# Optimization experiments

Measured on AMD Instinct MI355X. Metric: run time of the kernel, lower is better.

Reference implementation:

```python
import jax, jax.numpy as jnp
import numpy as np

D = 1024      # n_embd
NH = 16       # attention heads
E = 8         # n_experts
K = 2         # k_best
FF = 4 * D    # expert MLP hidden
EPS = 1e-6    # rms_norm_epsilon
TEMP = 1.0    # target_temperature


def setup_inputs() -> dict:
    key = jax.random.key(0)
    ks = jax.random.split(key, 12)
    B, S = 2, 1024
    s = 0.02
    return {
        "x": jax.random.normal(ks[0], (B, S, D), jnp.float32),
        "attn_norm_w": jnp.ones((D,), jnp.float32),
        "wq": jax.random.normal(ks[1], (D, D), jnp.float32) * s,
        "wk": jax.random.normal(ks[2], (D, D), jnp.float32) * s,
        "wv": jax.random.normal(ks[3], (D, D), jnp.float32) * s,
        "wo": jax.random.normal(ks[4], (D, D), jnp.float32) * s,
        "mlp_norm_w": jnp.ones((D,), jnp.float32),
        "router_w": jax.random.normal(ks[5], (D, E), jnp.float32) * s,
        "w1": jax.random.normal(ks[6], (E, D, FF), jnp.float32) * s,
        "b1": jnp.zeros((E, FF), jnp.float32),
        "w2": jax.random.normal(ks[7], (E, FF, D), jnp.float32) * s,
        "b2": jnp.zeros((E, D), jnp.float32),
    }


def _rmsnorm(x, w):
    var = jnp.mean(jnp.square(x), axis=-1, keepdims=True)
    return x * jax.lax.rsqrt(var + EPS) * w


def _attention(x, wq, wk, wv, wo):
    B, S, _ = x.shape
    dh = D // NH
    q = (x @ wq).reshape(B, S, NH, dh)
    k = (x @ wk).reshape(B, S, NH, dh)
    v = (x @ wv).reshape(B, S, NH, dh)
    scores = jnp.einsum("bqhd,bkhd->bhqk", q, k) / jnp.sqrt(jnp.float32(dh))
    causal = jnp.tril(jnp.ones((S, S), bool))  # [S,S]
    scores = jnp.where(causal[None, None], scores, jnp.finfo(scores.dtype).min)
    attn = jax.nn.softmax(scores, axis=-1)
    out = jnp.einsum("bhqk,bkhd->bqhd", attn, v).reshape(B, S, D)
    return out @ wo


def reference(x, attn_norm_w, wq, wk, wv, wo, mlp_norm_w, router_w, w1, b1, w2, b2):
    B, S, _ = x.shape
    # attention sub-block
    x = x + _attention(_rmsnorm(x, attn_norm_w), wq, wk, wv, wo)
    residual = x
    h = _rmsnorm(x, mlp_norm_w)  # [B,S,D]

    # router: temperature softmax + top-k
    logits = h @ router_w / TEMP                      # [B,S,E]
    probs = jax.nn.softmax(logits, axis=-1)
    top_k_scores, top_k_indices = jax.lax.top_k(probs, K)  # [B,S,K]
    onehot = jax.nn.one_hot(top_k_indices, E, dtype=h.dtype)  # [B,S,K,E]
    gates = jnp.einsum("bsk,bske->bse", top_k_scores, onehot)  # [B,S,E]

    # load-balancing loss (Switch-style) + expert counts
    counts = jnp.sum(onehot, axis=(0, 1, 2))          # [E]
    frac = counts / (B * S * K)
    mean_prob = jnp.mean(probs, axis=(0, 1))          # [E]
    balancing_loss = E * jnp.sum(frac * mean_prob)

    # experts: dense dispatch; tokens with zero gate contribute nothing,
    # so this matches the sort/gather/scatter top-k combine exactly.
    pre = jnp.einsum("bsd,edf->ebsf", h, w1) + b1[:, None, None]  # [E,B,S,FF]
    act = jax.nn.gelu(pre)
    y = jnp.einsum("ebsf,efd->ebsd", act, w2) + b2[:, None, None]  # [E,B,S,D]
    moe = jnp.einsum("ebsd,bse->bsd", y, gates)

    out = residual + moe
    return out, balancing_loss, counts
```

## Files before the change

kernel.cpp:

```cpp
#include <hip/hip_runtime.h>

typedef __bf16 bf16;
typedef __bf16 bf16x8 __attribute__((ext_vector_type(8)));
typedef float f32x4 __attribute__((ext_vector_type(4)));

#define D_   1024
#define S_   1024
#define B_   2
#define NTOK 2048
#define FF_  4096
#define NE   8
#define CAP  5120
#define OUTN 2097152

__device__ __forceinline__ float gelu_f(float x) {
    return 0.5f * x * (1.0f + tanhf(0.7978845608028654f * (x + 0.044715f * x * x * x)));
}

__global__ __launch_bounds__(256) void rmsnorm_k(const float* __restrict__ x,
                                                 const float* __restrict__ w,
                                                 float* __restrict__ yf,
                                                 bf16* __restrict__ yhi,
                                                 bf16* __restrict__ ylo) {
    int row = blockIdx.x;
    int t = threadIdx.x;
    const float* xr = x + (size_t)row * D_;
    float4 v = *(const float4*)(xr + t * 4);
    float ss = v.x * v.x + v.y * v.y + v.z * v.z + v.w * v.w;
    for (int off = 32; off; off >>= 1) ss += __shfl_down(ss, off);
    __shared__ float wsum[4];
    if ((t & 63) == 0) wsum[t >> 6] = ss;
    __syncthreads();
    float tot = wsum[0] + wsum[1] + wsum[2] + wsum[3];
    float rr = rsqrtf(tot * (1.0f / D_) + 1e-6f);
    float4 wv = *(const float4*)(w + t * 4);
    float y[4];
    y[0] = v.x * rr * wv.x; y[1] = v.y * rr * wv.y;
    y[2] = v.z * rr * wv.z; y[3] = v.w * rr * wv.w;
    if (yf) *(float4*)(yf + (size_t)row * D_ + t * 4) = *(float4*)y;
    if (yhi) {
#pragma unroll
        for (int i = 0; i < 4; i++) {
            bf16 hi = (bf16)y[i];
            yhi[(size_t)row * D_ + t * 4 + i] = hi;
            if (ylo) ylo[(size_t)row * D_ + t * 4 + i] = (bf16)(y[i] - (float)hi);
        }
    }
}

__global__ __launch_bounds__(256) void trans_split_k(
    const float* __restrict__ w0, const float* __restrict__ w1p,
    const float* __restrict__ w2p, const float* __restrict__ w3,
    bf16* o0h, bf16* o0l, bf16* o1h, bf16* o1l,
    bf16* o2h, bf16* o2l, bf16* o3h, bf16* o3l) {
    int z = blockIdx.z;
    const float* src = (z == 0) ? w0 : (z == 1) ? w1p : (z == 2) ? w2p : w3;
    bf16* dh = (z == 0) ? o0h : (z == 1) ? o1h : (z == 2) ? o2h : o3h;
    bf16* dl = (z == 0) ? o0l : (z == 1) ? o1l : (z == 2) ? o2l : o3l;
    __shared__ float tl[32][33];
    int c0 = blockIdx.x * 32, r0 = blockIdx.y * 32;
    int tx = threadIdx.x & 31, ty = threadIdx.x >> 5;
#pragma unroll
    for (int i = 0; i < 4; i++) {
        int r = ty + i * 8;
        tl[r][tx] = src[(size_t)(r0 + r) * 1024 + c0 + tx];
    }
    __syncthreads();
#pragma unroll
    for (int i = 0; i < 4; i++) {
        int c = ty + i * 8;
        float v = tl[tx][c];
        bf16 hi = (bf16)v;
        dh[(size_t)(c0 + c) * 1024 + r0 + tx] = hi;
        dl[(size_t)(c0 + c) * 1024 + r0 + tx] = (bf16)(v - (float)hi);
    }
}

__global__ __launch_bounds__(256) void transpose_cast_k(const float* __restrict__ in,
                                                        bf16* __restrict__ out,
                                                        int R, int C) {
    __shared__ float tl[32][33];
    size_t base = (size_t)blockIdx.z * R * C;
    const float* src = in + base;
    bf16* dst = out + base;
    int c0 = blockIdx.x * 32, r0 = blockIdx.y * 32;
    int tx = threadIdx.x & 31, tyy = threadIdx.x >> 5;
#pragma unroll
    for (int i = 0; i < 4; i++) {
        int r = tyy + i * 8;
        tl[r][tx] = src[(size_t)(r0 + r) * C + c0 + tx];
    }
    __syncthreads();
#pragma unroll
    for (int i = 0; i < 4; i++) {
        int c = tyy + i * 8;
        dst[(size_t)(c0 + c) * R + r0 + tx] = (bf16)tl[tx][c];
    }
}

#define GLD 40

#define GEMM64_SPLIT_BODY(N0EXPR, EPILOGUE)                                            \
    __shared__ bf16 Ash[64 * GLD], Asl[64 * GLD], Bsh[64 * GLD], Bsl[64 * GLD];        \
    int t = threadIdx.x;                                                               \
    int m0 = blockIdx.x * 64;                                                          \
    int n0 = (N0EXPR);                                                                 \
    int wv = t >> 6, ln = t & 63, l15 = ln & 15, qd = ln >> 4;                         \
    int srow = t >> 2, skc = (t & 3) * 8;                                              \
    f32x4 acc[4];                                                                      \
    _Pragma("unroll") for (int mt = 0; mt < 4; mt++) acc[mt] = (f32x4){0.f,0.f,0.f,0.f}; \
    for (int k0 = 0; k0 < 1024; k0 += 32) {                                            \
        __syncthreads();                                                               \
        *(bf16x8*)&Ash[srow * GLD + skc] = *(const bf16x8*)(Ah + (size_t)(m0 + srow) * 1024 + k0 + skc); \
        *(bf16x8*)&Asl[srow * GLD + skc] = *(const bf16x8*)(Al + (size_t)(m0 + srow) * 1024 + k0 + skc); \
        *(bf16x8*)&Bsh[srow * GLD + skc] = *(const bf16x8*)(Bh + (size_t)(n0 + srow) * 1024 + k0 + skc); \
        *(bf16x8*)&Bsl[srow * GLD + skc] = *(const bf16x8*)(Bl + (size_t)(n0 + srow) * 1024 + k0 + skc); \
        __syncthreads();                                                               \
        bf16x8 ah[4], al[4];                                                           \
        _Pragma("unroll") for (int mt = 0; mt < 4; mt++) {                             \
            ah[mt] = *(const bf16x8*)&Ash[(mt * 16 + l15) * GLD + qd * 8];             \
            al[mt] = *(const bf16x8*)&Asl[(mt * 16 + l15) * GLD + qd * 8];             \
        }                                                                              \
        bf16x8 bh = *(const bf16x8*)&Bsh[(wv * 16 + l15) * GLD + qd * 8];              \
        bf16x8 bl = *(const bf16x8*)&Bsl[(wv * 16 + l15) * GLD + qd * 8];              \
        _Pragma("unroll") for (int mt = 0; mt < 4; mt++) {                             \
            acc[mt] = __builtin_amdgcn_mfma_f32_16x16x32_bf16(ah[mt], bh, acc[mt], 0, 0, 0); \
            acc[mt] = __builtin_amdgcn_mfma_f32_16x16x32_bf16(ah[mt], bl, acc[mt], 0, 0, 0); \
            acc[mt] = __builtin_amdgcn_mfma_f32_16x16x32_bf16(al[mt], bh, acc[mt], 0, 0, 0); \
        }                                                                              \
    }                                                                                  \
    int gnl = wv * 16 + l15;                                                           \
    _Pragma("unroll") for (int mt = 0; mt < 4; mt++)                                   \
        _Pragma("unroll") for (int r = 0; r < 4; r++) {                                \
            int gm = m0 + mt * 16 + qd * 4 + r;                                        \
            float vv = acc[mt][r];                                                     \
            EPILOGUE                                                                   \
        }

__global__ __launch_bounds__(256) void gemm_qkv_k(
    const bf16* __restrict__ Ah, const bf16* __restrict__ Al,
    const bf16* __restrict__ Bqh, const bf16* __restrict__ Bql,
    const bf16* __restrict__ Bkh, const bf16* __restrict__ Bkl,
    const bf16* __restrict__ Bvh, const bf16* __restrict__ Bvl,
    bf16* Cqh, bf16* Cql, bf16* Ckh, bf16* Ckl, bf16* Cvh, bf16* Cvl) {
    int gy = blockIdx.y, zw = gy >> 4;
    const bf16* Bh = (zw == 0) ? Bqh : (zw == 1) ? Bkh : Bvh;
    const bf16* Bl = (zw == 0) ? Bql : (zw == 1) ? Bkl : Bvl;
    bf16* Ch = (zw == 0) ? Cqh : (zw == 1) ? Ckh : Cvh;
    bf16* Cl = (zw == 0) ? Cql : (zw == 1) ? Ckl : Cvl;
    GEMM64_SPLIT_BODY((gy & 15) * 64, {
        bf16 hi = (bf16)vv;
        Ch[(size_t)gm * D_ + n0 + gnl] = hi;
        Cl[(size_t)gm * D_ + n0 + gnl] = (bf16)(vv - (float)hi);
    })
}

__global__ __launch_bounds__(256) void gemm_wo_k(
    const bf16* __restrict__ Ah, const bf16* __restrict__ Al,
    const bf16* __restrict__ Bh, const bf16* __restrict__ Bl,
    float* __restrict__ C, const float* __restrict__ X) {
    GEMM64_SPLIT_BODY(blockIdx.y * 64, {
        C[(size_t)gm * D_ + n0 + gnl] = X[(size_t)gm * D_ + n0 + gnl] + vv;
    })
}

#define AP 72

__global__ __launch_bounds__(256) void attn_mfma_k(
    const bf16* __restrict__ qhp, const bf16* __restrict__ qlp,
    const bf16* __restrict__ khp, const bf16* __restrict__ klp,
    const bf16* __restrict__ vhp, const bf16* __restrict__ vlp,
    bf16* __restrict__ aoh, bf16* __restrict__ aol) {
    int qt = (int)gridDim.x - 1 - (int)blockIdx.x;
    int h = blockIdx.y, b = blockIdx.z;
    __shared__ bf16 Ksh[64 * AP], Ksl[64 * AP], VTh[64 * AP], VTl[64 * AP];
    __shared__ bf16 Ph[4][16 * AP], Pl[4][16 * AP];
    int t = threadIdx.x, wv = t >> 6, ln = t & 63, l15 = ln & 15, qd = ln >> 4;

    bf16x8 aqh[2], aql[2];
    {
        size_t qb = ((size_t)(b * S_ + qt * 64 + wv * 16 + l15)) * D_ + h * 64 + qd * 8;
        aqh[0] = *(const bf16x8*)(qhp + qb);
        aqh[1] = *(const bf16x8*)(qhp + qb + 32);
        aql[0] = *(const bf16x8*)(qlp + qb);
        aql[1] = *(const bf16x8*)(qlp + qb + 32);
    }
    f32x4 oacc[4];
    float mrow[4], lrow[4];
#pragma unroll
    for (int i = 0; i < 4; i++) {
        oacc[i] = (f32x4){0.f, 0.f, 0.f, 0.f};
        mrow[i] = -1e30f; lrow[i] = 0.0f;
    }

    for (int kt = 0; kt <= qt; kt++) {
        __syncthreads();
#pragma unroll
        for (int j = 0; j < 2; j++) {
            int idx = t + j * 256;
            int row = idx >> 3, ch = (idx & 7) * 8;
            size_t g = ((size_t)(b * S_ + kt * 64 + row)) * D_ + h * 64 + ch;
            *(bf16x8*)&Ksh[row * AP + ch] = *(const bf16x8*)(khp + g);
            *(bf16x8*)&Ksl[row * AP + ch] = *(const bf16x8*)(klp + g);
            bf16x8 vvh = *(const bf16x8*)(vhp + g);
            bf16x8 vvl = *(const bf16x8*)(vlp + g);
#pragma unroll
            for (int jj = 0; jj < 8; jj++) {
                VTh[(ch + jj) * AP + row] = vvh[jj];
                VTl[(ch + jj) * AP + row] = vvl[jj];
            }
        }
        __syncthreads();

        f32x4 sacc[4];
#pragma unroll
        for (int nt = 0; nt < 4; nt++) sacc[nt] = (f32x4){0.f, 0.f, 0.f, 0.f};
#pragma unroll
        for (int ks = 0; ks < 2; ks++) {
#pragma unroll
            for (int nt = 0; nt < 4; nt++) {
                bf16x8 bh = *(const bf16x8*)&Ksh[(nt * 16 + l15) * AP + ks * 32 + qd * 8];
                bf16x8 bl = *(const bf16x8*)&Ksl[(nt * 16 + l15) * AP + ks * 32 + qd * 8];
                sacc[nt] = __builtin_amdgcn_mfma_f32_16x16x32_bf16(aqh[ks], bh, sacc[nt], 0, 0, 0);
                sacc[nt] = __builtin_amdgcn_mfma_f32_16x16x32_bf16(aqh[ks], bl, sacc[nt], 0, 0, 0);
                sacc[nt] = __builtin_amdgcn_mfma_f32_16x16x32_bf16(aql[ks], bh, sacc[nt], 0, 0, 0);
            }
        }
        bool diag = (kt == qt);
#pragma unroll
        for (int r = 0; r < 4; r++) {
            float s0[4];
#pragma unroll
            for (int nt = 0; nt < 4; nt++) {
                s0[nt] = sacc[nt][r] * 0.125f;
                if (diag && (nt * 16 + l15) > (wv * 16 + qd * 4 + r)) s0[nt] = -1e30f;
            }
            float vmax = fmaxf(fmaxf(s0[0], s0[1]), fmaxf(s0[2], s0[3]));
            for (int off = 1; off < 16; off <<= 1) vmax = fmaxf(vmax, __shfl_xor(vmax, off));
            float mnew = fmaxf(mrow[r], vmax);
            float alpha = expf(mrow[r] - mnew);
            float p[4], rs = 0.0f;
#pragma unroll
            for (int nt = 0; nt < 4; nt++) { p[nt] = expf(s0[nt] - mnew); rs += p[nt]; }
            for (int off = 1; off < 16; off <<= 1) rs += __shfl_xor(rs, off);
            lrow[r] = lrow[r] * alpha + rs;
            mrow[r] = mnew;
#pragma unroll
            for (int nt = 0; nt < 4; nt++) oacc[nt][r] *= alpha;
            int prow = qd * 4 + r;
#pragma unroll
            for (int nt = 0; nt < 4; nt++) {
                bf16 hi = (bf16)p[nt];
                Ph[wv][prow * AP + nt * 16 + l15] = hi;
                Pl[wv][prow * AP + nt * 16 + l15] = (bf16)(p[nt] - (float)hi);
            }
        }
#pragma unroll
        for (int ks2 = 0; ks2 < 2; ks2++) {
            bf16x8 aph = *(const bf16x8*)&Ph[wv][l15 * AP + ks2 * 32 + qd * 8];
            bf16x8 apl = *(const bf16x8*)&Pl[wv][l15 * AP + ks2 * 32 + qd * 8];
#pragma unroll
            for (int nt = 0; nt < 4; nt++) {
                bf16x8 bvh = *(const bf16x8*)&VTh[(nt * 16 + l15) * AP + ks2 * 32 + qd * 8];
                bf16x8 bvl = *(const bf16x8*)&VTl[(nt * 16 + l15) * AP + ks2 * 32 + qd * 8];
                oacc[nt] = __builtin_amdgcn_mfma_f32_16x16x32_bf16(aph, bvh, oacc[nt], 0, 0, 0);
                oacc[nt] = __builtin_amdgcn_mfma_f32_16x16x32_bf16(aph, bvl, oacc[nt], 0, 0, 0);
                oacc[nt] = __builtin_amdgcn_mfma_f32_16x16x32_bf16(apl, bvh, oacc[nt], 0, 0, 0);
            }
        }
    }

#pragma unroll
    for (int r = 0; r < 4; r++) {
        float inv = 1.0f / lrow[r];
        size_t rowa = ((size_t)(b * S_ + qt * 64 + wv * 16 + qd * 4 + r)) * D_ + h * 64;
#pragma unroll
        for (int nt = 0; nt < 4; nt++) {
            float o = oacc[nt][r] * inv;
            bf16 hi = (bf16)o;
            aoh[rowa + nt * 16 + l15] = hi;
            aol[rowa + nt * 16 + l15] = (bf16)(o - (float)hi);
        }
    }
}

__global__ __launch_bounds__(256) void router_k(const float* __restrict__ h,
                                                const float* __restrict__ rw,
                                                int* __restrict__ tidx,
                                                float* __restrict__ tgate,
                                                int* __restrict__ ecnt,
                                                float* __restrict__ psum) {
    int wv = threadIdx.x >> 6, ln = threadIdx.x & 63;
    int tok = blockIdx.x * 4 + wv;
    const float* hr = h + (size_t)tok * D_;
    float acc[NE];
#pragma unroll
    for (int e = 0; e < NE; e++) acc[e] = 0.0f;
    int base = ln * 16;
#pragma unroll
    for (int c = 0; c < 4; c++) {
        float4 hv = *(const float4*)(hr + base + c * 4);
        const float* rp = rw + (size_t)(base + c * 4) * NE;
        float hx[4] = {hv.x, hv.y, hv.z, hv.w};
#pragma unroll
        for (int jj = 0; jj < 4; jj++)
#pragma unroll
            for (int e = 0; e < NE; e++)
                acc[e] = fmaf(hx[jj], rp[jj * NE + e], acc[e]);
    }
#pragma unroll
    for (int e = 0; e < NE; e++)
        for (int off = 32; off; off >>= 1) acc[e] += __shfl_down(acc[e], off);

    __shared__ float pb[4][NE];
    if (ln == 0) {
        float mx = acc[0];
#pragma unroll
        for (int e = 1; e < NE; e++) mx = fmaxf(mx, acc[e]);
        float p[NE], ssum = 0.0f;
#pragma unroll
        for (int e = 0; e < NE; e++) { p[e] = expf(acc[e] - mx); ssum += p[e]; }
        float inv = 1.0f / ssum;
#pragma unroll
        for (int e = 0; e < NE; e++) p[e] *= inv;
        int i0 = 0; float b0 = p[0];
#pragma unroll
        for (int e = 1; e < NE; e++) if (p[e] > b0) { b0 = p[e]; i0 = e; }
        int i1 = -1; float b1v = -1.0f;
#pragma unroll
        for (int e = 0; e < NE; e++) if (e != i0 && p[e] > b1v) { b1v = p[e]; i1 = e; }
        tidx[tok * 2] = i0; tidx[tok * 2 + 1] = i1;
        tgate[tok * 2] = b0; tgate[tok * 2 + 1] = b1v;
        atomicAdd(&ecnt[i0], 1);
        atomicAdd(&ecnt[i1], 1);
#pragma unroll
        for (int e = 0; e < NE; e++) pb[wv][e] = p[e];
    }
    __syncthreads();
    if (threadIdx.x < NE) {
        float s2 = pb[0][threadIdx.x] + pb[1][threadIdx.x] + pb[2][threadIdx.x] + pb[3][threadIdx.x];
        atomicAdd(&psum[threadIdx.x], s2);
    }
}

__global__ void passb_k(const int* __restrict__ ecnt, const float* __restrict__ psum,
                        int* __restrict__ eoffp, int* __restrict__ ecnt2,
                        float* __restrict__ out_tail) {
    if (threadIdx.x == 0) {
        int off = 0; float loss = 0.0f;
        for (int e = 0; e < NE; e++) {
            eoffp[e] = off;
            int c = ecnt[e];
            off += (c + 127) & ~127;
            loss += (c * (1.0f / 4096.0f)) * (psum[e] * (1.0f / 2048.0f));
            out_tail[1 + e] = (float)c;
            ecnt2[e] = 0;
        }
        eoffp[NE] = off;
        out_tail[0] = 8.0f * loss;
    }
}

__global__ __launch_bounds__(256) void scatter_k(const int* __restrict__ tidx,
                                                 const int* __restrict__ eoffp,
                                                 int* __restrict__ ecnt2,
                                                 int* __restrict__ stok,
                                                 int* __restrict__ sidx) {
    int tok = blockIdx.x * 256 + threadIdx.x;
    for (int k = 0; k < 2; k++) {
        int e = tidx[tok * 2 + k];
        int pos = eoffp[e] + atomicAdd(&ecnt2[e], 1);
        stok[pos] = tok;
        sidx[tok * 2 + k] = pos;
    }
}

#define MLD 40

__global__ __launch_bounds__(256) void moe_gemm1_k(const bf16* __restrict__ hB,
                                                   const bf16* __restrict__ w1t,
                                                   const float* __restrict__ b1,
                                                   const int* __restrict__ eoffp,
                                                   const int* __restrict__ stok,
                                                   bf16* __restrict__ act) {
    int m0 = blockIdx.x * 128, n0 = blockIdx.y * 128;
    if (m0 >= eoffp[NE]) return;
    int e = 0;
#pragma unroll
    for (int i = 1; i < NE; i++) if (m0 >= eoffp[i]) e = i;

    __shared__ bf16 As[128 * MLD];
    __shared__ bf16 Bs[128 * MLD];
    __shared__ int tok_l[128];
    int t = threadIdx.x;
    if (t < 128) tok_l[t] = stok[m0 + t];

    int wv = t >> 6, ln = t & 63;
    int wm = wv >> 1, wn = wv & 1;
    int lane15 = ln & 15, quad = ln >> 4;
    f32x4 acc[4][4];
#pragma unroll
    for (int mt = 0; mt < 4; mt++)
#pragma unroll
        for (int nt = 0; nt < 4; nt++) acc[mt][nt] = (f32x4){0.f, 0.f, 0.f, 0.f};

    const bf16* Bbase = w1t + ((size_t)e * FF_ + n0) * D_;

    for (int k0 = 0; k0 < D_; k0 += 32) {
        __syncthreads();
#pragma unroll
        for (int j = 0; j < 2; j++) {
            int idx = t + j * 256;
            int row = idx >> 2, kc = (idx & 3) * 8;
            uint4 av = *(const uint4*)(hB + (size_t)tok_l[row] * D_ + k0 + kc);
            *(uint4*)&As[row * MLD + kc] = av;
            uint4 bv = *(const uint4*)(Bbase + (size_t)row * D_ + k0 + kc);
            *(uint4*)&Bs[row * MLD + kc] = bv;
        }
        __syncthreads();
        bf16x8 af[4], bfr[4];
#pragma unroll
        for (int mt = 0; mt < 4; mt++)
            af[mt] = *(const bf16x8*)&As[(wm * 64 + mt * 16 + lane15) * MLD + quad * 8];
#pragma unroll
        for (int nt = 0; nt < 4; nt++)
            bfr[nt] = *(const bf16x8*)&Bs[(wn * 64 + nt * 16 + lane15) * MLD + quad * 8];
#pragma unroll
        for (int mt = 0; mt < 4; mt++)
#pragma unroll
            for (int nt = 0; nt < 4; nt++)
                acc[mt][nt] = __builtin_amdgcn_mfma_f32_16x16x32_bf16(af[mt], bfr[nt], acc[mt][nt], 0, 0, 0);
    }

    const float* b1e = b1 + (size_t)e * FF_;
#pragma unroll
    for (int mt = 0; mt < 4; mt++)
#pragma unroll
        for (int nt = 0; nt < 4; nt++) {
            int gn = n0 + wn * 64 + nt * 16 + lane15;
            float bias = b1e[gn];
#pragma unroll
            for (int r = 0; r < 4; r++) {
                int gm = m0 + wm * 64 + mt * 16 + quad * 4 + r;
                float vv = acc[mt][nt][r] + bias;
                act[(size_t)gm * FF_ + gn] = (bf16)gelu_f(vv);
            }
        }
}

__global__ __launch_bounds__(256) void moe_gemm2_k(const bf16* __restrict__ act,
                                                   const bf16* __restrict__ w2t,
                                                   const float* __restrict__ b2,
                                                   const int* __restrict__ eoffp,
                                                   float* __restrict__ y) {
    int m0 = blockIdx.x * 64;
    if (m0 >= eoffp[NE]) return;
    int e = 0;
#pragma unroll
    for (int i = 1; i < NE; i++) if (m0 >= eoffp[i]) e = i;
    int n0 = blockIdx.y * 64;

    __shared__ bf16 As[64 * MLD];
    __shared__ bf16 Bs[64 * MLD];
    int t = threadIdx.x;
    int wv = t >> 6, ln = t & 63, l15 = ln & 15, qd = ln >> 4;
    int srow = t >> 2, skc = (t & 3) * 8;

    f32x4 acc[4];
#pragma unroll
    for (int mt = 0; mt < 4; mt++) acc[mt] = (f32x4){0.f, 0.f, 0.f, 0.f};

    const bf16* Bbase = w2t + ((size_t)e * D_ + n0) * FF_;

    for (int k0 = 0; k0 < FF_; k0 += 32) {
        __syncthreads();
        *(bf16x8*)&As[srow * MLD + skc] = *(const bf16x8*)(act + (size_t)(m0 + srow) * FF_ + k0 + skc);
        *(bf16x8*)&Bs[srow * MLD + skc] = *(const bf16x8*)(Bbase + (size_t)srow * FF_ + k0 + skc);
        __syncthreads();
        bf16x8 af[4];
#pragma unroll
        for (int mt = 0; mt < 4; mt++)
            af[mt] = *(const bf16x8*)&As[(mt * 16 + l15) * MLD + qd * 8];
        bf16x8 bfr = *(const bf16x8*)&Bs[(wv * 16 + l15) * MLD + qd * 8];
#pragma unroll
        for (int mt = 0; mt < 4; mt++)
            acc[mt] = __builtin_amdgcn_mfma_f32_16x16x32_bf16(af[mt], bfr, acc[mt], 0, 0, 0);
    }

    int gn = n0 + wv * 16 + l15;
    float bias = b2[(size_t)e * D_ + gn];
#pragma unroll
    for (int mt = 0; mt < 4; mt++)
#pragma unroll
        for (int r = 0; r < 4; r++) {
            int gm = m0 + mt * 16 + qd * 4 + r;
            y[(size_t)gm * D_ + gn] = acc[mt][r] + bias;
        }
}

__global__ __launch_bounds__(256) void combine_k(const float* __restrict__ y,
                                                 const int* __restrict__ sidx,
                                                 const float* __restrict__ tgate,
                                                 float* __restrict__ out) {
    int tok = blockIdx.x;
    int d = threadIdx.x * 4;
    int s0 = sidx[tok * 2], s1 = sidx[tok * 2 + 1];
    float g0 = tgate[tok * 2], g1 = tgate[tok * 2 + 1];
    float4 a = *(const float4*)(y + (size_t)s0 * D_ + d);
    float4 b = *(const float4*)(y + (size_t)s1 * D_ + d);
    float4 o = *(const float4*)(out + (size_t)tok * D_ + d);
    o.x += g0 * a.x + g1 * b.x;
    o.y += g0 * a.y + g1 * b.y;
    o.z += g0 * a.z + g1 * b.z;
    o.w += g0 * a.w + g1 * b.w;
    *(float4*)(out + (size_t)tok * D_ + d) = o;
}

extern "C" void kernel_launch(void* const* d_in, const int* in_sizes, int n_in,
                              void* d_out, int out_size, void* d_ws, size_t ws_size,
                              hipStream_t stream) {
    const float* x   = (const float*)d_in[0];
    const float* anw = (const float*)d_in[1];
    const float* wq  = (const float*)d_in[2];
    const float* wk  = (const float*)d_in[3];
    const float* wv  = (const float*)d_in[4];
    const float* wo  = (const float*)d_in[5];
    const float* mnw = (const float*)d_in[6];
    const float* rw  = (const float*)d_in[7];
    const float* w1  = (const float*)d_in[8];
    const float* b1  = (const float*)d_in[9];
    const float* w2  = (const float*)d_in[10];
    const float* b2  = (const float*)d_in[11];
    float* out = (float*)d_out;

    char* p = (char*)d_ws;
    auto take = [&](size_t n) { char* r = p; p += (n + 255) & ~(size_t)255; return r; };
    bf16* h1h = (bf16*)take((size_t)OUTN * 2);
    bf16* h1l = (bf16*)take((size_t)OUTN * 2);
    bf16* qh  = (bf16*)take((size_t)OUTN * 2);
    bf16* ql  = (bf16*)take((size_t)OUTN * 2);
    bf16* kh  = (bf16*)take((size_t)OUTN * 2);
    bf16* kl  = (bf16*)take((size_t)OUTN * 2);
    bf16* vh  = (bf16*)take((size_t)OUTN * 2);
    bf16* vl  = (bf16*)take((size_t)OUTN * 2);
    bf16* wqth = (bf16*)take((size_t)D_ * D_ * 2);
    bf16* wqtl = (bf16*)take((size_t)D_ * D_ * 2);
    bf16* wkth = (bf16*)take((size_t)D_ * D_ * 2);
    bf16* wktl = (bf16*)take((size_t)D_ * D_ * 2);
    bf16* wvth = (bf16*)take((size_t)D_ * D_ * 2);
    bf16* wvtl = (bf16*)take((size_t)D_ * D_ * 2);
    bf16* woth = (bf16*)take((size_t)D_ * D_ * 2);
    bf16* wotl = (bf16*)take((size_t)D_ * D_ * 2);
    bf16* w1t = (bf16*)take((size_t)NE * FF_ * D_ * 2);
    bf16* w2t = (bf16*)take((size_t)NE * FF_ * D_ * 2);
    bf16* act = (bf16*)take((size_t)CAP * FF_ * 2);
    int*   tidx  = (int*)take(NTOK * 2 * 4);
    float* tgate = (float*)take(NTOK * 2 * 4);
    int*   sidx  = (int*)take(NTOK * 2 * 4);
    int*   ecnt  = (int*)take(64);
    int*   ecnt2 = (int*)take(64);
    float* psum  = (float*)take(64);
    int*   eoffp = (int*)take(64);
    int*   stok  = (int*)take(CAP * 4);

    bf16*  aoh = h1h;
    bf16*  aol = h1l;
    float* h_f = (float*)qh;
    bf16*  h_b = kh;
    float* y   = (float*)vh;

    hipMemsetAsync(ecnt, 0, NE * 4, stream);
    hipMemsetAsync(psum, 0, NE * 4, stream);
    hipMemsetAsync(stok, 0, CAP * 4, stream);

    trans_split_k<<<dim3(32, 32, 4), 256, 0, stream>>>(wq, wk, wv, wo,
        wqth, wqtl, wkth, wktl, wvth, wvtl, woth, wotl);
    transpose_cast_k<<<dim3(FF_ / 32, D_ / 32, NE), 256, 0, stream>>>(w1, w1t, D_, FF_);
    transpose_cast_k<<<dim3(D_ / 32, FF_ / 32, NE), 256, 0, stream>>>(w2, w2t, FF_, D_);

    rmsnorm_k<<<NTOK, 256, 0, stream>>>(x, anw, nullptr, h1h, h1l);
    gemm_qkv_k<<<dim3(32, 48), 256, 0, stream>>>(h1h, h1l,
        wqth, wqtl, wkth, wktl, wvth, wvtl, qh, ql, kh, kl, vh, vl);
    attn_mfma_k<<<dim3(16, 16, 2), 256, 0, stream>>>(qh, ql, kh, kl, vh, vl, aoh, aol);
    gemm_wo_k<<<dim3(32, 16), 256, 0, stream>>>(aoh, aol, woth, wotl, out, x);

    rmsnorm_k<<<NTOK, 256, 0, stream>>>(out, mnw, h_f, h_b, nullptr);
    router_k<<<NTOK / 4, 256, 0, stream>>>(h_f, rw, tidx, tgate, ecnt, psum);
    passb_k<<<1, 64, 0, stream>>>(ecnt, psum, eoffp, ecnt2, out + OUTN);
    scatter_k<<<NTOK / 256, 256, 0, stream>>>(tidx, eoffp, ecnt2, stok, sidx);
    moe_gemm1_k<<<dim3(CAP / 128, FF_ / 128), 256, 0, stream>>>(h_b, w1t, b1, eoffp, stok, act);
    moe_gemm2_k<<<dim3(CAP / 64, D_ / 64), 256, 0, stream>>>(act, w2t, b2, eoffp, y);
    combine_k<<<NTOK, 256, 0, stream>>>(y, sidx, tgate, out);
}
```

Before: 838.6 us.

## Use direct global-to-LDS loads with XOR swizzle and enlarge MoE GEMM2 tiles

Both MoE GEMMs now stage A/B tiles with global_load_lds (direct-to-LDS 16-byte loads) into unpadded 32-wide LDS rows, using an XOR swizzle on the column chunk to avoid bank conflicts instead of padding. GEMM2 is retiled from 64x64 blocks with 4 MFMAs per wave to 128x128 blocks with a 4x4 MFMA grid per wave, raising arithmetic intensity and data reuse. This removes the register round trip for tile staging but changes the grid size, so fewer blocks run for GEMM2. The global_load_lds layout assumes a specific lane-to-LDS mapping, which carries some correctness risk.

```diff
diff --git a/kernel.cpp b/kernel.cpp
--- a/kernel.cpp
+++ b/kernel.cpp
@@ -15,6 +15,12 @@
 
 __device__ __forceinline__ float gelu_f(float x) {
     return 0.5f * x * (1.0f + tanhf(0.7978845608028654f * (x + 0.044715f * x * x * x)));
+}
+
+__device__ __forceinline__ void gload16(const void* g, void* l) {
+    __builtin_amdgcn_global_load_lds((const __attribute__((address_space(1))) unsigned int*)g,
+                                     (__attribute__((address_space(3))) unsigned int*)l,
+                                     16, 0, 0);
 }
 
 __global__ __launch_bounds__(256) void rmsnorm_k(const float* __restrict__ x,
@@ -375,8 +381,6 @@
     }
 }
 
-#define MLD 40
-
 __global__ __launch_bounds__(256) void moe_gemm1_k(const bf16* __restrict__ hB,
                                                    const bf16* __restrict__ w1t,
                                                    const float* __restrict__ b1,
@@ -389,42 +393,51 @@
 #pragma unroll
     for (int i = 1; i < NE; i++) if (m0 >= eoffp[i]) e = i;
 
-    __shared__ bf16 As[128 * MLD];
-    __shared__ bf16 Bs[128 * MLD];
-    __shared__ int tok_l[128];
+    __shared__ __align__(16) bf16 As[128 * 32];
+    __shared__ __align__(16) bf16 Bs[128 * 32];
     int t = threadIdx.x;
-    if (t < 128) tok_l[t] = stok[m0 + t];
-
     int wv = t >> 6, ln = t & 63;
-    int wm = wv >> 1, wn = wv & 1;
-    int lane15 = ln & 15, quad = ln >> 4;
+    int wm = wv >> 1, wn = wv & 1, l15 = ln & 15, qd = ln >> 4;
+
+    int sr0 = t >> 2, sr1 = 64 + sr0, cl = t & 3;
+    int cs0 = (cl ^ ((sr0 >> 1) & 3)) * 8;
+    int cs1 = (cl ^ ((sr1 >> 1) & 3)) * 8;
+    const bf16* ga0 = hB + (size_t)stok[m0 + sr0] * D_ + cs0;
+    const bf16* ga1 = hB + (size_t)stok[m0 + sr1] * D_ + cs1;
+    const bf16* Bb = w1t + ((size_t)e * FF_ + n0) * D_;
+    const bf16* gb0 = Bb + (size_t)sr0 * D_ + cs0;
+    const bf16* gb1 = Bb + (size_t)sr1 * D_ + cs1;
+    bf16* lA0 = As + wv * 512;  bf16* lA1 = As + 2048 + wv * 512;
+    bf16* lB0 = Bs + wv * 512;  bf16* lB1 = Bs + 2048 + wv * 512;
+
+    const bf16 *ra[4], *rb[4];
+#pragma unroll
+    for (int i = 0; i < 4; i++) {
+        int r1 = wm * 64 + i * 16 + l15;
+        ra[i] = As + r1 * 32 + (qd ^ ((r1 >> 1) & 3)) * 8;
+        int r2 = wn * 64 + i * 16 + l15;
+        rb[i] = Bs + r2 * 32 + (qd ^ ((r2 >> 1) & 3)) * 8;
+    }
+
     f32x4 acc[4][4];
 #pragma unroll
     for (int mt = 0; mt < 4; mt++)
 #pragma unroll
         for (int nt = 0; nt < 4; nt++) acc[mt][nt] = (f32x4){0.f, 0.f, 0.f, 0.f};
-
-    const bf16* Bbase = w1t + ((size_t)e * FF_ + n0) * D_;
 
     for (int k0 = 0; k0 < D_; k0 += 32) {
         __syncthreads();
-#pragma unroll
-        for (int j = 0; j < 2; j++) {
-            int idx = t + j * 256;
-            int row = idx >> 2, kc = (idx & 3) * 8;
-            uint4 av = *(const uint4*)(hB + (size_t)tok_l[row] * D_ + k0 + kc);
-            *(uint4*)&As[row * MLD + kc] = av;
-            uint4 bv = *(const uint4*)(Bbase + (size_t)row * D_ + k0 + kc);
-            *(uint4*)&Bs[row * MLD + kc] = bv;
-        }
+        gload16(ga0 + k0, lA0);
+        gload16(ga1 + k0, lA1);
+        gload16(gb0 + k0, lB0);
+        gload16(gb1 + k0, lB1);
         __syncthreads();
         bf16x8 af[4], bfr[4];
 #pragma unroll
-        for (int mt = 0; mt < 4; mt++)
-            af[mt] = *(const bf16x8*)&As[(wm * 64 + mt * 16 + lane15) * MLD + quad * 8];
-#pragma unroll
-        for (int nt = 0; nt < 4; nt++)
-            bfr[nt] = *(const bf16x8*)&Bs[(wn * 64 + nt * 16 + lane15) * MLD + quad * 8];
+        for (int i = 0; i < 4; i++) {
+            af[i] = *(const bf16x8*)ra[i];
+            bfr[i] = *(const bf16x8*)rb[i];
+        }
 #pragma unroll
         for (int mt = 0; mt < 4; mt++)
 #pragma unroll
@@ -437,13 +450,12 @@
     for (int mt = 0; mt < 4; mt++)
 #pragma unroll
         for (int nt = 0; nt < 4; nt++) {
-            int gn = n0 + wn * 64 + nt * 16 + lane15;
+            int gn = n0 + wn * 64 + nt * 16 + l15;
             float bias = b1e[gn];
 #pragma unroll
             for (int r = 0; r < 4; r++) {
-                int gm = m0 + wm * 64 + mt * 16 + quad * 4 + r;
-                float vv = acc[mt][nt][r] + bias;
-                act[(size_t)gm * FF_ + gn] = (bf16)gelu_f(vv);
+                int gm = m0 + wm * 64 + mt * 16 + qd * 4 + r;
+                act[(size_t)gm * FF_ + gn] = (bf16)gelu_f(acc[mt][nt][r] + bias);
             }
         }
 }
@@ -453,48 +465,76 @@
                                                    const float* __restrict__ b2,
                                                    const int* __restrict__ eoffp,
                                                    float* __restrict__ y) {
-    int m0 = blockIdx.x * 64;
+    int m0 = blockIdx.x * 128, n0 = blockIdx.y * 128;
     if (m0 >= eoffp[NE]) return;
     int e = 0;
 #pragma unroll
     for (int i = 1; i < NE; i++) if (m0 >= eoffp[i]) e = i;
-    int n0 = blockIdx.y * 64;
-
-    __shared__ bf16 As[64 * MLD];
-    __shared__ bf16 Bs[64 * MLD];
+
+    __shared__ __align__(16) bf16 As[128 * 32];
+    __shared__ __align__(16) bf16 Bs[128 * 32];
     int t = threadIdx.x;
-    int wv = t >> 6, ln = t & 63, l15 = ln & 15, qd = ln >> 4;
-    int srow = t >> 2, skc = (t & 3) * 8;
-
-    f32x4 acc[4];
-#pragma unroll
-    for (int mt = 0; mt < 4; mt++) acc[mt] = (f32x4){0.f, 0.f, 0.f, 0.f};
-
-    const bf16* Bbase = w2t + ((size_t)e * D_ + n0) * FF_;
+    int wv = t >> 6, ln = t & 63;
+    int wm = wv >> 1, wn = wv & 1, l15 = ln & 15, qd = ln >> 4;
+
+    int sr0 = t >> 2, sr1 = 64 + sr0, cl = t & 3;
+    int cs0 = (cl ^ ((sr0 >> 1) & 3)) * 8;
+    int cs1 = (cl ^ ((sr1 >> 1) & 3)) * 8;
+    const bf16* ga0 = act + (size_t)(m0 + sr0) * FF_ + cs0;
+    const bf16* ga1 = act + (size_t)(m0 + sr1) * FF_ + cs1;
+    const bf16* Bb = w2t + ((size_t)e * D_ + n0) * FF_;
+    const bf16* gb0 = Bb + (size_t)sr0 * FF_ + cs0;
+    const bf16* gb1 = Bb + (size_t)sr1 * FF_ + cs1;
+    bf16* lA0 = As + wv * 512;  bf16* lA1 = As + 2048 + wv * 512;
+    bf16* lB0 = Bs + wv * 512;  bf16* lB1 = Bs + 2048 + wv * 512;
+
+    const bf16 *ra[4], *rb[4];
+#pragma unroll
+    for (int i = 0; i < 4; i++) {
+        int r1 = wm * 64 + i * 16 + l15;
+        ra[i] = As + r1 * 32 + (qd ^ ((r1 >> 1) & 3)) * 8;
+        int r2 = wn * 64 + i * 16 + l15;
+        rb[i] = Bs + r2 * 32 + (qd ^ ((r2 >> 1) & 3)) * 8;
+    }
+
+    f32x4 acc[4][4];
+#pragma unroll
+    for (int mt = 0; mt < 4; mt++)
+#pragma unroll
+        for (int nt = 0; nt < 4; nt++) acc[mt][nt] = (f32x4){0.f, 0.f, 0.f, 0.f};
 
     for (int k0 = 0; k0 < FF_; k0 += 32) {
         __syncthreads();
-        *(bf16x8*)&As[srow * MLD + skc] = *(const bf16x8*)(act + (size_t)(m0 + srow) * FF_ + k0 + skc);
-        *(bf16x8*)&Bs[srow * MLD + skc] = *(const bf16x8*)(Bbase + (size_t)srow * FF_ + k0 + skc);
+        gload16(ga0 + k0, lA0);
+        gload16(ga1 + k0, lA1);
+        gload16(gb0 + k0, lB0);
+        gload16(gb1 + k0, lB1);
         __syncthreads();
-        bf16x8 af[4];
+        bf16x8 af[4], bfr[4];
+#pragma unroll
+        for (int i = 0; i < 4; i++) {
+            af[i] = *(const bf16x8*)ra[i];
+            bfr[i] = *(const bf16x8*)rb[i];
+        }
 #pragma unroll
         for (int mt = 0; mt < 4; mt++)
-            af[mt] = *(const bf16x8*)&As[(mt * 16 + l15) * MLD + qd * 8];
-        bf16x8 bfr = *(const bf16x8*)&Bs[(wv * 16 + l15) * MLD + qd * 8];
-#pragma unroll
-        for (int mt = 0; mt < 4; mt++)
-            acc[mt] = __builtin_amdgcn_mfma_f32_16x16x32_bf16(af[mt], bfr, acc[mt], 0, 0, 0);
-    }
-
-    int gn = n0 + wv * 16 + l15;
-    float bias = b2[(size_t)e * D_ + gn];
+#pragma unroll
+            for (int nt = 0; nt < 4; nt++)
+                acc[mt][nt] = __builtin_amdgcn_mfma_f32_16x16x32_bf16(af[mt], bfr[nt], acc[mt][nt], 0, 0, 0);
+    }
+
+    const float* b2e = b2 + (size_t)e * D_;
 #pragma unroll
     for (int mt = 0; mt < 4; mt++)
 #pragma unroll
-        for (int r = 0; r < 4; r++) {
-            int gm = m0 + mt * 16 + qd * 4 + r;
-            y[(size_t)gm * D_ + gn] = acc[mt][r] + bias;
+        for (int nt = 0; nt < 4; nt++) {
+            int gn = n0 + wn * 64 + nt * 16 + l15;
+            float bias = b2e[gn];
+#pragma unroll
+            for (int r = 0; r < 4; r++) {
+                int gm = m0 + wm * 64 + mt * 16 + qd * 4 + r;
+                y[(size_t)gm * D_ + gn] = acc[mt][nt][r] + bias;
+            }
         }
 }
 
@@ -589,6 +629,6 @@
     passb_k<<<1, 64, 0, stream>>>(ecnt, psum, eoffp, ecnt2, out + OUTN);
     scatter_k<<<NTOK / 256, 256, 0, stream>>>(tidx, eoffp, ecnt2, stok, sidx);
     moe_gemm1_k<<<dim3(CAP / 128, FF_ / 128), 256, 0, stream>>>(h_b, w1t, b1, eoffp, stok, act);
-    moe_gemm2_k<<<dim3(CAP / 64, D_ / 64), 256, 0, stream>>>(act, w2t, b2, eoffp, y);
+    moe_gemm2_k<<<dim3(CAP / 128, D_ / 128), 256, 0, stream>>>(act, w2t, b2, eoffp, y);
     combine_k<<<NTOK, 256, 0, stream>>>(y, sidx, tgate, out);
 }
```

Result: faster. 787.2 us (-6.1%).
